# Kernel optimization log

Hardware: AMD Instinct MI355X
Metric: run time of the kernel (lower is better)

Reference implementation:

```python
import jax, jax.numpy as jnp
import numpy as np

B, C, IMG, P = 256, 1, 256, 32
GRID = IMG // P              # 8 (matches attention defaults image_size=64/patch_size=8 -> 8x8 grid)
NPATCH = GRID * GRID         # 64
N = NPATCH + 1               # 65 tokens incl. cls
D, HEADS, DEPTH, F = 1024, 16, 12, 4096
HD = D // HEADS              # 64
D2 = HD // 2                 # 32
SEQ = 8                      # RoPE cache length from attention defaults (64//8)
EPS = 1e-5
SCALE = HD ** -0.5


def build_rope(seq_len, d):
    inv = 1.0 / (10000.0 ** (jnp.arange(0, d, 2, dtype=jnp.float32) / d))
    t = jnp.arange(seq_len, dtype=jnp.float32)
    f = jnp.outer(t, inv)                       # [seq, d//2]
    return jnp.repeat(jnp.cos(f), 2, axis=-1), jnp.repeat(jnp.sin(f), 2, axis=-1)


def layernorm(x, g, b):
    mu = jnp.mean(x, axis=-1, keepdims=True)
    var = jnp.mean(jnp.square(x - mu), axis=-1, keepdims=True)
    return (x - mu) * jax.lax.rsqrt(var + EPS) * g + b


def apply_rope(x, cos, sin):
    # x: [B,H,N,d2]; cos/sin: [N,d2] (broadcast)
    xe, xo = x[..., ::2], x[..., 1::2]
    xr = jnp.stack([-xo, xe], axis=-1).reshape(x.shape)
    return x * cos + xr * sin


def setup_inputs() -> dict:
    key = jax.random.key(0)
    ks = jax.random.split(key, 16)
    s = 0.02
    inp = {
        "img": jax.random.normal(ks[0], (B, C, IMG, IMG), jnp.float32),
        "patch_W": jax.random.normal(ks[1], (P * P * C, D), jnp.float32) * s,
        "patch_b": jnp.zeros((D,), jnp.float32),
        "cls_token": jax.random.normal(ks[2], (1, 1, D), jnp.float32),
        "ln1_g": jnp.ones((DEPTH, D), jnp.float32),
        "ln1_b": jnp.zeros((DEPTH, D), jnp.float32),
        "Wqkv": jax.random.normal(ks[3], (DEPTH, D, 3 * D), jnp.float32) * s,
        "Wproj": jax.random.normal(ks[4], (DEPTH, D, D), jnp.float32) * s,
        "bproj": jnp.zeros((DEPTH, D), jnp.float32),
        "ln2_g": jnp.ones((DEPTH, D), jnp.float32),
        "ln2_b": jnp.zeros((DEPTH, D), jnp.float32),
        "W1": jax.random.normal(ks[5], (DEPTH, D, F), jnp.float32) * s,
        "b1": jnp.zeros((DEPTH, F), jnp.float32),
        "W2": jax.random.normal(ks[6], (DEPTH, F, D), jnp.float32) * s,
        "b2": jnp.zeros((DEPTH, D), jnp.float32),
        "lnf_g": jnp.ones((D,), jnp.float32),
        "lnf_b": jnp.zeros((D,), jnp.float32),
    }
    return inp


def reference(img, patch_W, patch_b, cls_token, ln1_g, ln1_b, Wqkv, Wproj, bproj,
              ln2_g, ln2_b, W1, b1, W2, b2, lnf_g, lnf_b):
    Bn = img.shape[0]
    # Patch embed: b c (h p1) (w p2) -> b (h w) (p1 p2 c)
    x = img.reshape(Bn, C, GRID, P, GRID, P).transpose(0, 2, 4, 3, 5, 1)
    x = x.reshape(Bn, NPATCH, P * P * C) @ patch_W + patch_b
    cls = jnp.broadcast_to(cls_token, (Bn, 1, D))
    x = jnp.concatenate([cls, x], axis=1)  # [B,N,D]; NOTE: pos_embedding is unused in original

    # 2D RoPE caches (attention-internal defaults: 8x8 grid)
    cos_row, sin_row = build_rope(SEQ, D2)
    cos_col, sin_col = build_rope(SEQ, D2)
    lin = jnp.arange(NPATCH)
    row_ids = jnp.concatenate([jnp.zeros(1, jnp.int32), (lin // SEQ).astype(jnp.int32)])
    col_ids = jnp.concatenate([jnp.zeros(1, jnp.int32), (lin % SEQ).astype(jnp.int32)])
    cos_r, sin_r = cos_row[row_ids], sin_row[row_ids]   # [N,D2]
    cos_c, sin_c = cos_col[col_ids], sin_col[col_ids]

    def block(x, p):
        g1, bb1n, Wq, Wp, bp, g2, bb2n, w1, bv1, w2, bv2 = p
        h = layernorm(x, g1, bb1n)
        qkv = (h @ Wq).reshape(Bn, N, 3, HEADS, HD).transpose(2, 0, 3, 1, 4)
        q, k, v = qkv[0], qkv[1], qkv[2]            # [B,H,N,HD]
        q = jnp.concatenate([apply_rope(q[..., :D2], cos_r, sin_r),
                             apply_rope(q[..., D2:], cos_c, sin_c)], axis=-1)
        k = jnp.concatenate([apply_rope(k[..., :D2], cos_r, sin_r),
                             apply_rope(k[..., D2:], cos_c, sin_c)], axis=-1)
        attn = jax.nn.softmax(jnp.einsum('bhnd,bhmd->bhnm', q, k) * SCALE, axis=-1)
        o = jnp.einsum('bhnm,bhmd->bhnd', attn, v).transpose(0, 2, 1, 3).reshape(Bn, N, D)
        x = x + o @ Wp + bp
        h2 = layernorm(x, g2, bb2n)
        h2 = jax.nn.gelu(h2 @ w1 + bv1, approximate=False)
        x = x + h2 @ w2 + bv2
        return x, None

    x, _ = jax.lax.scan(block, x, (ln1_g, ln1_b, Wqkv, Wproj, bproj, ln2_g, ln2_b, W1, b1, W2, b2))
    x = layernorm(x, lnf_g, lnf_b)
    return x[:, 0]
```

## Files before the change

kernel.cpp:

```cpp
#include <hip/hip_runtime.h>
#include <hip/hip_bf16.h>
#include <math.h>

using bf16 = __hip_bfloat16;
typedef __bf16 bf16x8 __attribute__((ext_vector_type(8)));
typedef float f32x4 __attribute__((ext_vector_type(4)));

#define NTOK 65
#define BATCH 256
#define DIM 1024
#define NROWS (BATCH * NTOK)
#define FDIM 4096
#define NHEADS 16
#define NLAYER 12

__device__ __forceinline__ float b2f(bf16 v) { return __bfloat162float(v); }
__device__ __forceinline__ bf16 f2b(float v) { return __float2bfloat16(v); }

__device__ __forceinline__ void load16(const void* g, void* l) {
  __builtin_amdgcn_global_load_lds((const __attribute__((address_space(1))) void*)g,
                                   (__attribute__((address_space(3))) void*)l,
                                   16, 0, 0);
}

__global__ __launch_bounds__(256) void transpose_w(const float* __restrict__ W,
                                                   bf16* __restrict__ Wt, int K, int Nn) {
  __shared__ float t[32][33];
  int l = blockIdx.z;
  const float* Wl = W + (size_t)l * K * Nn;
  bf16* Wtl = Wt + (size_t)l * K * Nn;
  int n0 = blockIdx.x * 32, k0 = blockIdx.y * 32;
  int tx = threadIdx.x, ty = threadIdx.y;
  for (int i = 0; i < 4; i++)
    t[ty + i * 8][tx] = Wl[(size_t)(k0 + ty + i * 8) * Nn + n0 + tx];
  __syncthreads();
  for (int i = 0; i < 4; i++)
    Wtl[(size_t)(n0 + ty + i * 8) * K + k0 + tx] = f2b(t[tx][ty + i * 8]);
}

__global__ __launch_bounds__(256) void im2col_k(const float* __restrict__ img, bf16* __restrict__ out) {
  int idx = blockIdx.x * 256 + threadIdx.x;
  int c = idx & 31, r = (idx >> 5) & 31, p = (idx >> 10) & 63, b = idx >> 16;
  int gr = p >> 3, gc = p & 7;
  out[idx] = f2b(img[((size_t)b << 16) + (size_t)(gr * 32 + r) * 256 + gc * 32 + c]);
}

__global__ __launch_bounds__(256) void clsfill_k(const float* __restrict__ cls, float* __restrict__ xbuf) {
  int idx = blockIdx.x * 256 + threadIdx.x;
  int b = idx >> 10, d = idx & 1023;
  xbuf[(size_t)(b * NTOK) * DIM + d] = cls[d];
}

__global__ __launch_bounds__(256) void ln_k(const float* __restrict__ x, const float* __restrict__ g,
                                            const float* __restrict__ bt, bf16* __restrict__ out) {
  int row = blockIdx.x;
  int t = threadIdx.x;
  float4 v = ((const float4*)(x + (size_t)row * DIM))[t];
  float s = v.x + v.y + v.z + v.w;
  float ss = v.x * v.x + v.y * v.y + v.z * v.z + v.w * v.w;
  for (int off = 32; off > 0; off >>= 1) { s += __shfl_down(s, off, 64); ss += __shfl_down(ss, off, 64); }
  __shared__ float sh[8];
  int w = t >> 6, lane = t & 63;
  if (lane == 0) { sh[w] = s; sh[w + 4] = ss; }
  __syncthreads();
  s = sh[0] + sh[1] + sh[2] + sh[3];
  ss = sh[4] + sh[5] + sh[6] + sh[7];
  float mu = s * (1.f / DIM);
  float rs = rsqrtf(ss * (1.f / DIM) - mu * mu + 1e-5f);
  float4 gv = ((const float4*)g)[t];
  float4 bv = ((const float4*)bt)[t];
  bf16* o = out + (size_t)row * DIM + t * 4;
  o[0] = f2b((v.x - mu) * rs * gv.x + bv.x);
  o[1] = f2b((v.y - mu) * rs * gv.y + bv.y);
  o[2] = f2b((v.z - mu) * rs * gv.z + bv.z);
  o[3] = f2b((v.w - mu) * rs * gv.w + bv.w);
}

__global__ __launch_bounds__(256) void lnf_k(const float* __restrict__ x, const float* __restrict__ g,
                                             const float* __restrict__ bt, float* __restrict__ out) {
  int b = blockIdx.x;
  int t = threadIdx.x;
  float4 v = ((const float4*)(x + (size_t)(b * NTOK) * DIM))[t];
  float s = v.x + v.y + v.z + v.w;
  float ss = v.x * v.x + v.y * v.y + v.z * v.z + v.w * v.w;
  for (int off = 32; off > 0; off >>= 1) { s += __shfl_down(s, off, 64); ss += __shfl_down(ss, off, 64); }
  __shared__ float sh[8];
  int w = t >> 6, lane = t & 63;
  if (lane == 0) { sh[w] = s; sh[w + 4] = ss; }
  __syncthreads();
  s = sh[0] + sh[1] + sh[2] + sh[3];
  ss = sh[4] + sh[5] + sh[6] + sh[7];
  float mu = s * (1.f / DIM);
  float rs = rsqrtf(ss * (1.f / DIM) - mu * mu + 1e-5f);
  float4 gv = ((const float4*)g)[t];
  float4 bv = ((const float4*)bt)[t];
  float4 o;
  o.x = (v.x - mu) * rs * gv.x + bv.x;
  o.y = (v.y - mu) * rs * gv.y + bv.y;
  o.z = (v.z - mu) * rs * gv.z + bv.z;
  o.w = (v.w - mu) * rs * gv.w + bv.w;
  ((float4*)(out + (size_t)b * DIM))[t] = o;
}

template <int MODE>
__global__ __launch_bounds__(256) void gemm_bt(const bf16* __restrict__ A, const bf16* __restrict__ Bt,
                                               const float* __restrict__ bias, const float* __restrict__ res,
                                               float* __restrict__ outf, bf16* __restrict__ outb,
                                               int M, int Nn, int K) {
  __shared__ __align__(16) bf16 As[128 * 32];
  __shared__ __align__(16) bf16 Bs[128 * 32];
  int tid = threadIdx.x;
  int w = tid >> 6, lane = tid & 63;
  int quad = lane >> 4, lr = lane & 15;
  int m0 = blockIdx.y * 128, n0 = blockIdx.x * 128;
  int srow = w * 32 + (lane >> 2);
  int skoff = (lane & 3) * 8;
  const bf16* Ag = A + (size_t)(m0 + srow) * K + skoff;
  const bf16* Bg = Bt + (size_t)(n0 + srow) * K + skoff;
  bf16* AsW = &As[w * 1024];
  bf16* BsW = &Bs[w * 1024];
  int wm = (w >> 1) * 64, wn = (w & 1) * 64;
  f32x4 acc[4][4];
  for (int i = 0; i < 4; i++)
    for (int j = 0; j < 4; j++) acc[i][j] = (f32x4){0.f, 0.f, 0.f, 0.f};
  for (int kb = 0; kb < K; kb += 32) {
    load16(Ag + kb, AsW);
    load16(Ag + kb + (size_t)16 * K, AsW + 512);
    load16(Bg + kb, BsW);
    load16(Bg + kb + (size_t)16 * K, BsW + 512);
    __syncthreads();
    bf16x8 af[4], bfr[4];
    for (int i = 0; i < 4; i++)
      af[i] = *reinterpret_cast<const bf16x8*>(&As[(wm + i * 16 + lr) * 32 + quad * 8]);
    for (int i = 0; i < 4; i++)
      bfr[i] = *reinterpret_cast<const bf16x8*>(&Bs[(wn + i * 16 + lr) * 32 + quad * 8]);
    for (int mi = 0; mi < 4; mi++)
      for (int ni = 0; ni < 4; ni++)
        acc[mi][ni] = __builtin_amdgcn_mfma_f32_16x16x32_bf16(af[mi], bfr[ni], acc[mi][ni], 0, 0, 0);
    __syncthreads();
  }
  for (int mi = 0; mi < 4; mi++)
    for (int ni = 0; ni < 4; ni++)
      for (int r = 0; r < 4; r++) {
        int grow = m0 + wm + mi * 16 + quad * 4 + r;
        int gcol = n0 + wn + ni * 16 + lr;
        float v = acc[mi][ni][r];
        if (MODE == 0) {
          outb[(size_t)grow * Nn + gcol] = f2b(v);
        } else if (MODE == 1) {
          v += bias[gcol];
          v = 0.5f * v * (1.f + erff(v * 0.70710678118f));
          outb[(size_t)grow * Nn + gcol] = f2b(v);
        } else if (MODE == 2) {
          size_t o = (size_t)grow * Nn + gcol;
          outf[o] = res[o] + v + bias[gcol];
        } else {
          int prow = grow + (grow >> 6) + 1;
          outf[(size_t)prow * DIM + gcol] = v + bias[gcol];
        }
      }
}

__global__ __launch_bounds__(256) void attn_k(const bf16* __restrict__ qkv, bf16* __restrict__ O) {
  int bh = blockIdx.x;
  int b = bh >> 4, hh = bh & 15;
  __shared__ __align__(16) bf16 Qs[80 * 64];
  __shared__ __align__(16) bf16 Ks[80 * 64];
  __shared__ __align__(16) bf16 Vt[64 * 104];
  __shared__ __align__(16) bf16 Pb[80 * 96];
  __shared__ float Sc[80 * 81];
  int tid = threadIdx.x;
  const bf16* base = qkv + (size_t)(b * NTOK) * 3072 + hh * 64;
  for (int idx = tid; idx < NTOK * 32; idx += 256) {
    int n = idx >> 5, p = idx & 31;
    int j = p & 15;
    int pos = (n == 0) ? 0 : ((p < 16) ? ((n - 1) >> 3) : ((n - 1) & 7));
    float inv = __powf(10000.f, -(float)j * (1.f / 16.f));
    float ang = (float)pos * inv;
    float cs = __cosf(ang), sn = __sinf(ang);
    const bf16* qp = base + (size_t)n * 3072 + 2 * p;
    float qe = b2f(qp[0]), qo = b2f(qp[1]);
    Qs[n * 64 + 2 * p] = f2b(qe * cs - qo * sn);
    Qs[n * 64 + 2 * p + 1] = f2b(qo * cs + qe * sn);
    const bf16* kp = qp + 1024;
    float ke = b2f(kp[0]), ko = b2f(kp[1]);
    Ks[n * 64 + 2 * p] = f2b(ke * cs - ko * sn);
    Ks[n * 64 + 2 * p + 1] = f2b(ko * cs + ke * sn);
  }
  for (int idx = tid; idx < NTOK * 64; idx += 256) {
    int m = idx >> 6, d = idx & 63;
    Vt[d * 104 + m] = base[(size_t)m * 3072 + 2048 + d];
  }
  for (int i = tid; i < 64 * 39; i += 256) {
    int d = i / 39, m = 65 + i % 39;
    Vt[d * 104 + m] = f2b(0.f);
  }
  __syncthreads();
  int w = tid >> 6, lane = tid & 63, quad = lane >> 4, lr = lane & 15;
  for (int t = w; t < 25; t += 4) {
    int mi = t / 5, ni = t % 5;
    f32x4 c = (f32x4){0.f, 0.f, 0.f, 0.f};
    for (int ks = 0; ks < 2; ks++) {
      bf16x8 aq = *reinterpret_cast<const bf16x8*>(&Qs[(mi * 16 + lr) * 64 + ks * 32 + quad * 8]);
      bf16x8 bk = *reinterpret_cast<const bf16x8*>(&Ks[(ni * 16 + lr) * 64 + ks * 32 + quad * 8]);
      c = __builtin_amdgcn_mfma_f32_16x16x32_bf16(aq, bk, c, 0, 0, 0);
    }
    for (int r = 0; r < 4; r++)
      Sc[(mi * 16 + quad * 4 + r) * 81 + ni * 16 + lr] = c[r] * 0.125f;
  }
  __syncthreads();
  if (tid < 80) {
    bf16* pr = &Pb[tid * 96];
    if (tid < NTOK) {
      float* row = &Sc[tid * 81];
      float mx = row[0];
      for (int m = 1; m < NTOK; m++) mx = fmaxf(mx, row[m]);
      float sum = 0.f;
      for (int m = 0; m < NTOK; m++) {
        float e = __expf(row[m] - mx);
        row[m] = e;
        sum += e;
      }
      float is = 1.f / sum;
      for (int m = 0; m < NTOK; m++) pr[m] = f2b(row[m] * is);
      for (int m = NTOK; m < 96; m++) pr[m] = f2b(0.f);
    } else {
      for (int m = 0; m < 96; m++) pr[m] = f2b(0.f);
    }
  }
  __syncthreads();
  for (int t = w; t < 20; t += 4) {
    int mi = t >> 2, di = t & 3;
    f32x4 c = (f32x4){0.f, 0.f, 0.f, 0.f};
    for (int ks = 0; ks < 3; ks++) {
      bf16x8 ap = *reinterpret_cast<const bf16x8*>(&Pb[(mi * 16 + lr) * 96 + ks * 32 + quad * 8]);
      bf16x8 bv = *reinterpret_cast<const bf16x8*>(&Vt[(di * 16 + lr) * 104 + ks * 32 + quad * 8]);
      c = __builtin_amdgcn_mfma_f32_16x16x32_bf16(ap, bv, c, 0, 0, 0);
    }
    for (int r = 0; r < 4; r++) {
      int n = mi * 16 + quad * 4 + r;
      if (n < NTOK)
        O[(size_t)(b * NTOK + n) * DIM + hh * 64 + di * 16 + lr] = f2b(c[r]);
    }
  }
}

extern "C" void kernel_launch(void* const* d_in, const int* in_sizes, int n_in,
                              void* d_out, int out_size, void* d_ws, size_t ws_size,
                              hipStream_t stream) {
  const float* img = (const float*)d_in[0];
  const float* patch_W = (const float*)d_in[1];
  const float* patch_b = (const float*)d_in[2];
  const float* cls_token = (const float*)d_in[3];
  const float* ln1_g = (const float*)d_in[4];
  const float* ln1_b = (const float*)d_in[5];
  const float* Wqkv = (const float*)d_in[6];
  const float* Wproj = (const float*)d_in[7];
  const float* bproj = (const float*)d_in[8];
  const float* ln2_g = (const float*)d_in[9];
  const float* ln2_b = (const float*)d_in[10];
  const float* W1 = (const float*)d_in[11];
  const float* b1 = (const float*)d_in[12];
  const float* W2 = (const float*)d_in[13];
  const float* b2 = (const float*)d_in[14];
  const float* lnf_g = (const float*)d_in[15];
  const float* lnf_b = (const float*)d_in[16];
  float* out = (float*)d_out;

  char* ws = (char*)d_ws;
  size_t off = 0;
  auto alloc = [&](size_t bytes) -> void* {
    void* p = ws + off;
    off += (bytes + 255) & ~(size_t)255;
    return p;
  };
  bf16* wt_patch = (bf16*)alloc((size_t)2 * 1024 * 1024);
  bf16* wt_qkv = (bf16*)alloc((size_t)2 * NLAYER * 1024 * 3072);
  bf16* wt_proj = (bf16*)alloc((size_t)2 * NLAYER * 1024 * 1024);
  bf16* wt_w1 = (bf16*)alloc((size_t)2 * NLAYER * 1024 * 4096);
  bf16* wt_w2 = (bf16*)alloc((size_t)2 * NLAYER * 1024 * 4096);
  float* xbuf = (float*)alloc((size_t)4 * NROWS * DIM);
  bf16* bufA = (bf16*)alloc((size_t)2 * NROWS * DIM);
  bf16* bufB = (bf16*)alloc((size_t)2 * NROWS * FDIM);
  if (off > ws_size) return;

  dim3 tb(32, 8);
  transpose_w<<<dim3(32, 32, 1), tb, 0, stream>>>(patch_W, wt_patch, 1024, 1024);
  transpose_w<<<dim3(96, 32, NLAYER), tb, 0, stream>>>(Wqkv, wt_qkv, 1024, 3072);
  transpose_w<<<dim3(32, 32, NLAYER), tb, 0, stream>>>(Wproj, wt_proj, 1024, 1024);
  transpose_w<<<dim3(128, 32, NLAYER), tb, 0, stream>>>(W1, wt_w1, 1024, 4096);
  transpose_w<<<dim3(32, 128, NLAYER), tb, 0, stream>>>(W2, wt_w2, 4096, 1024);

  im2col_k<<<65536, 256, 0, stream>>>(img, bufB);
  clsfill_k<<<1024, 256, 0, stream>>>(cls_token, xbuf);
  gemm_bt<3><<<dim3(8, 128), 256, 0, stream>>>(bufB, wt_patch, patch_b, nullptr, xbuf, nullptr,
                                               16384, 1024, 1024);

  for (int l = 0; l < NLAYER; l++) {
    ln_k<<<NROWS, 256, 0, stream>>>(xbuf, ln1_g + l * DIM, ln1_b + l * DIM, bufA);
    gemm_bt<0><<<dim3(24, 130), 256, 0, stream>>>(bufA, wt_qkv + (size_t)l * 3072 * 1024, nullptr,
                                                  nullptr, nullptr, bufB, NROWS, 3072, 1024);
    attn_k<<<BATCH * NHEADS, 256, 0, stream>>>(bufB, bufA);
    gemm_bt<2><<<dim3(8, 130), 256, 0, stream>>>(bufA, wt_proj + (size_t)l * 1024 * 1024,
                                                 bproj + l * DIM, xbuf, xbuf, nullptr, NROWS, 1024, 1024);
    ln_k<<<NROWS, 256, 0, stream>>>(xbuf, ln2_g + l * DIM, ln2_b + l * DIM, bufA);
    gemm_bt<1><<<dim3(32, 130), 256, 0, stream>>>(bufA, wt_w1 + (size_t)l * 4096 * 1024,
                                                  b1 + l * FDIM, nullptr, nullptr, bufB, NROWS, 4096, 1024);
    gemm_bt<2><<<dim3(8, 130), 256, 0, stream>>>(bufB, wt_w2 + (size_t)l * 4096 * 1024,
                                                 b2 + l * DIM, xbuf, xbuf, nullptr, NROWS, 1024, 4096);
  }
  lnf_k<<<BATCH, 256, 0, stream>>>(xbuf, lnf_g, lnf_b, out);
}
```

Before: 11.37 ms.

## Double K-step per barrier, swizzle block order, and use fast erf in GELU

The GEMM kernel now loads two 32-wide K slices per iteration into doubled LDS buffers, which halves the number of barrier pairs per K loop. Block indices are remapped into groups of 32 row-tiles so that concurrently running blocks share B tiles in L2. The GELU epilogue replaces erff with an Abramowitz-Stegun polynomial plus __expf. The trade-offs are higher LDS use per block, which may lower occupancy, and slightly lower erf accuracy.

New measurement: 10.40 ms. -8.5%, faster.

```diff
diff --git a/kernel.cpp b/kernel.cpp
--- a/kernel.cpp
+++ b/kernel.cpp
@@ -21,6 +21,17 @@
   __builtin_amdgcn_global_load_lds((const __attribute__((address_space(1))) void*)g,
                                    (__attribute__((address_space(3))) void*)l,
                                    16, 0, 0);
+}
+
+__device__ __forceinline__ float fast_erf(float x) {
+  float ax = fabsf(x);
+  float t = 1.f / (1.f + 0.3275911f * ax);
+  float y = t * (0.254829592f +
+            t * (-0.284496736f +
+            t * (1.421413741f +
+            t * (-1.453152027f + t * 1.061405429f))));
+  float r = 1.f - y * __expf(-ax * ax);
+  return copysignf(r, x);
 }
 
 __global__ __launch_bounds__(256) void transpose_w(const float* __restrict__ W,
@@ -107,12 +118,23 @@
                                                const float* __restrict__ bias, const float* __restrict__ res,
                                                float* __restrict__ outf, bf16* __restrict__ outb,
                                                int M, int Nn, int K) {
-  __shared__ __align__(16) bf16 As[128 * 32];
-  __shared__ __align__(16) bf16 Bs[128 * 32];
+  __shared__ __align__(16) bf16 As[2 * 128 * 32];
+  __shared__ __align__(16) bf16 Bs[2 * 128 * 32];
   int tid = threadIdx.x;
   int w = tid >> 6, lane = tid & 63;
   int quad = lane >> 4, lr = lane & 15;
-  int m0 = blockIdx.y * 128, n0 = blockIdx.x * 128;
+
+  int gx = gridDim.x, gy = gridDim.y;
+  int lin = blockIdx.y * gx + blockIdx.x;
+  const int T = 32;
+  int group = T * gx;
+  int g = lin / group;
+  int r = lin - g * group;
+  int rows = min(T, gy - g * T);
+  int tyy = g * T + r % rows;
+  int txx = r / rows;
+  int m0 = tyy * 128, n0 = txx * 128;
+
   int srow = w * 32 + (lane >> 2);
   int skoff = (lane & 3) * 8;
   const bf16* Ag = A + (size_t)(m0 + srow) * K + skoff;
@@ -123,33 +145,48 @@
   f32x4 acc[4][4];
   for (int i = 0; i < 4; i++)
     for (int j = 0; j < 4; j++) acc[i][j] = (f32x4){0.f, 0.f, 0.f, 0.f};
-  for (int kb = 0; kb < K; kb += 32) {
+
+  for (int kb = 0; kb < K; kb += 64) {
     load16(Ag + kb, AsW);
     load16(Ag + kb + (size_t)16 * K, AsW + 512);
     load16(Bg + kb, BsW);
     load16(Bg + kb + (size_t)16 * K, BsW + 512);
+    load16(Ag + kb + 32, AsW + 4096);
+    load16(Ag + kb + 32 + (size_t)16 * K, AsW + 4096 + 512);
+    load16(Bg + kb + 32, BsW + 4096);
+    load16(Bg + kb + 32 + (size_t)16 * K, BsW + 4096 + 512);
     __syncthreads();
-    bf16x8 af[4], bfr[4];
-    for (int i = 0; i < 4; i++)
-      af[i] = *reinterpret_cast<const bf16x8*>(&As[(wm + i * 16 + lr) * 32 + quad * 8]);
-    for (int i = 0; i < 4; i++)
-      bfr[i] = *reinterpret_cast<const bf16x8*>(&Bs[(wn + i * 16 + lr) * 32 + quad * 8]);
-    for (int mi = 0; mi < 4; mi++)
-      for (int ni = 0; ni < 4; ni++)
-        acc[mi][ni] = __builtin_amdgcn_mfma_f32_16x16x32_bf16(af[mi], bfr[ni], acc[mi][ni], 0, 0, 0);
+#pragma unroll
+    for (int h = 0; h < 2; h++) {
+      bf16x8 af[4], bfr[4];
+      const bf16* Ah = &As[h * 4096];
+      const bf16* Bh = &Bs[h * 4096];
+#pragma unroll
+      for (int i = 0; i < 4; i++)
+        af[i] = *reinterpret_cast<const bf16x8*>(&Ah[(wm + i * 16 + lr) * 32 + quad * 8]);
+#pragma unroll
+      for (int i = 0; i < 4; i++)
+        bfr[i] = *reinterpret_cast<const bf16x8*>(&Bh[(wn + i * 16 + lr) * 32 + quad * 8]);
+#pragma unroll
+      for (int mi = 0; mi < 4; mi++)
+#pragma unroll
+        for (int ni = 0; ni < 4; ni++)
+          acc[mi][ni] = __builtin_amdgcn_mfma_f32_16x16x32_bf16(af[mi], bfr[ni], acc[mi][ni], 0, 0, 0);
+    }
     __syncthreads();
   }
+
   for (int mi = 0; mi < 4; mi++)
     for (int ni = 0; ni < 4; ni++)
-      for (int r = 0; r < 4; r++) {
-        int grow = m0 + wm + mi * 16 + quad * 4 + r;
+      for (int rr = 0; rr < 4; rr++) {
+        int grow = m0 + wm + mi * 16 + quad * 4 + rr;
         int gcol = n0 + wn + ni * 16 + lr;
-        float v = acc[mi][ni][r];
+        float v = acc[mi][ni][rr];
         if (MODE == 0) {
           outb[(size_t)grow * Nn + gcol] = f2b(v);
         } else if (MODE == 1) {
           v += bias[gcol];
-          v = 0.5f * v * (1.f + erff(v * 0.70710678118f));
+          v = 0.5f * v * (1.f + fast_erf(v * 0.70710678118f));
           outb[(size_t)grow * Nn + gcol] = f2b(v);
         } else if (MODE == 2) {
           size_t o = (size_t)grow * Nn + gcol;
```
